# Kernel optimization log

Measured on AMD Instinct MI355X. Metric: run time of the kernel, lower is better.

## Reference

```python
import jax, jax.numpy as jnp
from jax import lax
import numpy as np

# correlation hyperparams (from init_kwargs)
MAX_D = 32      # maxDisplacement
PAD = 1         # zero padding
K = 3           # patch (kernel) size
STRIDE_K = 1    # stride over output pixels
STRIDE_D = 1    # stride over displacements


def setup_inputs() -> dict:
    key = jax.random.key(0)
    k0, k1 = jax.random.split(key)
    x0 = jax.random.normal(k0, (4, 64, 256, 512), dtype=jnp.float32)
    x1 = jax.random.normal(k1, (4, 64, 256, 512), dtype=jnp.float32)
    return {"x0": x0, "x1": x1}


def _corr2d(x0, x1):
    # x0, x1: [B, C, H, W] NCHW feature maps
    B, C, H, W = x0.shape
    # zero-pad spatially; x1 gets extra width padding so all displacements are in-bounds
    x0p = jnp.pad(x0, ((0, 0), (0, 0), (PAD, PAD), (PAD, PAD)))
    x1p = jnp.pad(x1, ((0, 0), (0, 0), (PAD, PAD), (PAD + MAX_D, PAD + MAX_D)))
    Wp = W + 2 * PAD
    # width offsets into x1p for displacements d = -MAX_D .. MAX_D step STRIDE_D
    offsets = jnp.arange(0, 2 * MAX_D + 1, STRIDE_D, dtype=jnp.int32)

    def step(carry, off):
        x1s = lax.dynamic_slice_in_dim(x1p, off, Wp, axis=3)   # [B,C,Hp,Wp]
        prod = jnp.sum(x0p * x1s, axis=1)                      # channel dot -> [B,Hp,Wp]
        # KxK box-sum over the patch, stride STRIDE_K -> [B,Ho,Wo]
        s = lax.reduce_window(prod, jnp.float32(0), lax.add,
                              (1, K, K), (1, STRIDE_K, STRIDE_K), 'VALID')
        return carry, s

    _, out = lax.scan(step, None, offsets)        # [nD, B, Ho, Wo]
    out = jnp.transpose(out, (1, 0, 2, 3))        # [B, nD, Ho, Wo]
    return out / jnp.asarray(K * K * C, out.dtype)


def reference(x0, x1):
    return _corr2d(x0, x1)
```

## Files before the change

### kernel.cpp

```cpp
#include <hip/hip_runtime.h>

#define WF 512
#define HF 256
#define CF 64
#define NDTOT 65
#define DP 72

static constexpr size_t CH  = (size_t)HF * WF;
static constexpr size_t WH  = (size_t)HF * WF;
static constexpr float  INV = 1.0f / 576.0f;

typedef _Float16 f16;
typedef _Float16 f16x4 __attribute__((ext_vector_type(4)));
typedef _Float16 f16x8 __attribute__((ext_vector_type(8)));
typedef float    f32x4 __attribute__((ext_vector_type(4)));

#if __has_builtin(__builtin_amdgcn_mfma_f32_16x16x16f16)
#define MFMA16(A, B, C) __builtin_amdgcn_mfma_f32_16x16x16f16((A), (B), (C), 0, 0, 0)
#define FRAG_T f16x4
__device__ __forceinline__ f16x4 mkfrag(f16 a, f16 b, f16 c, f16 d) {
    f16x4 r; r[0] = a; r[1] = b; r[2] = c; r[3] = d; return r;
}
#else
#define MFMA16(A, B, C) __builtin_amdgcn_mfma_f32_16x16x32_f16((A), (B), (C), 0, 0, 0)
#define FRAG_T f16x8
__device__ __forceinline__ f16x8 mkfrag(f16 a, f16 b, f16 c, f16 d) {
    f16x8 r; r[0] = a; r[1] = b; r[2] = c; r[3] = d;
    r[4] = (f16)0.f; r[5] = (f16)0.f; r[6] = (f16)0.f; r[7] = (f16)0.f; return r;
}
#endif

#define GLOADF(dst, ptr, offbytes) \
    asm volatile("global_load_dword %0, %1, %2" \
                 : "=v"(dst) : "v"(offbytes), "s"(ptr))

__global__ __launch_bounds__(256) __attribute__((amdgpu_waves_per_eu(3)))
void corr_gram(const float* __restrict__ x0, const float* __restrict__ x1,
               f16* __restrict__ ws) {
    const int f = blockIdx.x;
    const int tid = (f & 7) * 512 + (f >> 3);
    const int b = tid >> 10;
    const int y = (tid >> 2) & 255;
    const int sg = tid & 3;

    const int t = threadIdx.x;
    const int l = t & 63;
    const int w = t >> 6;
    const int xs = (sg * 4 + w) * 32;
    const int jb = xs - 32;

    const int n  = l & 15;
    const int kq = l >> 4;

    __shared__ f16 ebs[4][2304];

    const float* x0r = x0 + (size_t)b * CF * CH + (size_t)y * WF;
    const float* x1r = x1 + (size_t)b * CF * CH + (size_t)y * WF;

    int aB[2];
#pragma unroll
    for (int xt = 0; xt < 2; ++xt)
        aB[xt] = (4 * kq * (int)CH + xs + 16 * xt + n) * 4;
    int bB[6]; bool okj[6];
#pragma unroll
    for (int jt = 0; jt < 6; ++jt) {
        int col = jb + 16 * jt + n;
        okj[jt] = (unsigned)col < (unsigned)WF;
        col = col < 0 ? 0 : (col > 511 ? 511 : col);
        bB[jt] = (4 * kq * (int)CH + col) * 4;
    }

    f32x4 acc[10];
#pragma unroll
    for (int i = 0; i < 10; ++i) acc[i] = (f32x4)0.0f;

    float bufs[8][8];
    FRAG_T ah0, ah1, al0, al1;

#define ISS_A(kk, B) do { \
    _Pragma("unroll") for (int xt = 0; xt < 2; ++xt) \
    _Pragma("unroll") for (int i = 0; i < 4; ++i) \
        GLOADF(bufs[B][4*xt+i], x0r, aB[xt] + (16*(kk)+i) * (int)(CH*4)); \
    __builtin_amdgcn_sched_barrier(0); \
} while (0)

#define ISS_B(kk, p, B) do { \
    _Pragma("unroll") for (int u = 0; u < 2; ++u) \
    _Pragma("unroll") for (int i = 0; i < 4; ++i) \
        GLOADF(bufs[B][4*u+i], x1r, bB[2*((p)-1)+u] + (16*(kk)+i) * (int)(CH*4)); \
    __builtin_amdgcn_sched_barrier(0); \
} while (0)

#define WAITN(N) do { asm volatile("s_waitcnt vmcnt(" #N ")" ::: "memory"); \
                      __builtin_amdgcn_sched_barrier(0); } while (0)

#define TRIPLE(ai, AH, AL) do { \
    acc[ai] = MFMA16(AH, bh, acc[ai]); \
    acc[ai] = MFMA16(AH, bl, acc[ai]); \
    acc[ai] = MFMA16(AL, bh, acc[ai]); } while (0)

#define CON_A(B) do { \
    { const float v0 = bufs[B][0], v1 = bufs[B][1], v2 = bufs[B][2], v3 = bufs[B][3]; \
      const f16 h0 = (f16)v0, h1 = (f16)v1, h2 = (f16)v2, h3 = (f16)v3; \
      ah0 = mkfrag(h0, h1, h2, h3); \
      al0 = mkfrag((f16)(v0-(float)h0), (f16)(v1-(float)h1), (f16)(v2-(float)h2), (f16)(v3-(float)h3)); } \
    { const float v0 = bufs[B][4], v1 = bufs[B][5], v2 = bufs[B][6], v3 = bufs[B][7]; \
      const f16 h0 = (f16)v0, h1 = (f16)v1, h2 = (f16)v2, h3 = (f16)v3; \
      ah1 = mkfrag(h0, h1, h2, h3); \
      al1 = mkfrag((f16)(v0-(float)h0), (f16)(v1-(float)h1), (f16)(v2-(float)h2), (f16)(v3-(float)h3)); } \
} while (0)

#define CON_B(p, B) do { \
    _Pragma("unroll") for (int u = 0; u < 2; ++u) { \
        const int jt = 2*((p)-1) + u; \
        float v0 = bufs[B][4*u], v1 = bufs[B][4*u+1], v2 = bufs[B][4*u+2], v3 = bufs[B][4*u+3]; \
        v0 = okj[jt] ? v0 : 0.f; v1 = okj[jt] ? v1 : 0.f; \
        v2 = okj[jt] ? v2 : 0.f; v3 = okj[jt] ? v3 : 0.f; \
        const f16 h0 = (f16)v0, h1 = (f16)v1, h2 = (f16)v2, h3 = (f16)v3; \
        const FRAG_T bh = mkfrag(h0, h1, h2, h3); \
        const FRAG_T bl = mkfrag((f16)(v0-(float)h0), (f16)(v1-(float)h1), \
                                 (f16)(v2-(float)h2), (f16)(v3-(float)h3)); \
        if (jt < 5)  TRIPLE(jt, ah0, al0); \
        if (jt >= 1) TRIPLE(4 + jt, ah1, al1); \
    } \
} while (0)

    ISS_A(0, 0); ISS_B(0, 1, 1); ISS_B(0, 2, 2); ISS_B(0, 3, 3);
    ISS_A(1, 4); ISS_B(1, 1, 5); ISS_B(1, 2, 6);

    WAITN(48); ISS_B(1, 3, 7); CON_A(0);
    WAITN(48); ISS_A(2, 0);    CON_B(1, 1);
    WAITN(48); ISS_B(2, 1, 1); CON_B(2, 2);
    WAITN(48); ISS_B(2, 2, 2); CON_B(3, 3);
    WAITN(48); ISS_B(2, 3, 3); CON_A(4);
    WAITN(48); ISS_A(3, 4);    CON_B(1, 5);
    WAITN(48); ISS_B(3, 1, 5); CON_B(2, 6);
    WAITN(48); ISS_B(3, 2, 6); CON_B(3, 7);
    WAITN(48); ISS_B(3, 3, 7); CON_A(0);
    WAITN(48); CON_B(1, 1);
    WAITN(40); CON_B(2, 2);
    WAITN(32); CON_B(3, 3);
    WAITN(24); CON_A(4);
    WAITN(16); CON_B(1, 5);
    WAITN(8);  CON_B(2, 6);
    WAITN(0);  CON_B(3, 7);

#undef CON_B
#undef CON_A
#undef TRIPLE
#undef WAITN
#undef ISS_B
#undef ISS_A

    f16* eb = ebs[w];
#pragma unroll
    for (int xt = 0; xt < 2; ++xt) {
#pragma unroll
        for (int p = 0; p < 5; ++p) {
            const int i = xt * 5 + p;
#pragma unroll
            for (int q = 0; q < 4; ++q) {
                const int m = kq * 4 + q;
                const int xl = xt * 16 + m;
                const int d = 16 * p + n - m;
                if ((unsigned)d < (unsigned)NDTOT)
                    eb[xl * DP + d] = (f16)acc[i][q];
            }
        }
    }
#pragma unroll
    for (int i = 0; i < 4; ++i) {
        const int idx = l + 64 * i;
        if (idx < 224) {
            const int xl = idx / 7;
            eb[xl * DP + NDTOT + (idx - 7 * xl)] = (f16)0.f;
        }
    }
    uint4* dst = (uint4*)(ws + ((size_t)(b * HF + y) * WF + xs) * DP);
    const uint4* src = (const uint4*)eb;
#pragma unroll
    for (int i = 0; i < 5; ++i) {
        const int idx = l + 64 * i;
        if (idx < 288) dst[idx] = src[idx];
    }
}

__global__ __launch_bounds__(256)
void corr_box(const f16* __restrict__ ws, float* __restrict__ out) {
    const int xt = blockIdx.x;
    const int yt = blockIdx.y;
    const int b = blockIdx.z;
    const int t = threadIdx.x;
    const int x0b = xt * 32, y0 = yt * 8;

    __shared__ f16 S[10 * 34][DP];

    for (int u = 0; u < 10; ++u) {
        const int yy = y0 - 1 + u;
        const bool yok = (unsigned)yy < (unsigned)HF;
        const f16* src = ws + ((size_t)(b * HF + yy) * WF + (x0b - 1)) * DP;
#pragma unroll
        for (int sub = 0; sub < 2; ++sub) {
            const int idx = sub * 256 + t;
            if (idx < 306) {
                const int v = idx / 9, dg = idx - v * 9;
                const int xx = x0b - 1 + v;
                f16x8 val;
#pragma unroll
                for (int jj = 0; jj < 8; ++jj) val[jj] = (f16)0.f;
                if (yok && (unsigned)xx < (unsigned)WF)
                    val = *(const f16x8*)(src + (size_t)v * DP + dg * 8);
                *(f16x8*)&S[u * 34 + v][dg * 8] = val;
            }
        }
    }
    __syncthreads();

    const int ly = t >> 5, lx = t & 31;
    const int yg = y0 + ly, xg = x0b + lx;
    float* o0 = out + (size_t)b * NDTOT * WH + (size_t)yg * WF + xg;

#pragma unroll 1
    for (int dg = 0; dg < 9; ++dg) {
        f16x8 s;
#pragma unroll
        for (int jj = 0; jj < 8; ++jj) s[jj] = (f16)0.f;
#pragma unroll
        for (int du = 0; du < 3; ++du)
#pragma unroll
            for (int dv = 0; dv < 3; ++dv)
                s += *(const f16x8*)&S[(ly + du) * 34 + (lx + dv)][dg * 8];
#pragma unroll
        for (int jj = 0; jj < 8; ++jj) {
            const int d = dg * 8 + jj;
            if (d < NDTOT) o0[(size_t)d * WH] = (float)s[jj] * INV;
        }
    }
}

__global__ void corr_naive(const float* __restrict__ x0, const float* __restrict__ x1,
                           float* __restrict__ out) {
    const size_t total = (size_t)4 * NDTOT * WH;
    size_t idx = (size_t)blockIdx.x * blockDim.x + threadIdx.x;
    if (idx >= total) return;
    const int j = (int)(idx % WF);
    const int i = (int)((idx / WF) % HF);
    const int d = (int)((idx / WH) % NDTOT);
    const int b = (int)(idx / ((size_t)NDTOT * WH));
    const int disp = d - 32;
    float s = 0.f;
    for (int u = i - 1; u <= i + 1; ++u) {
        if (u < 0 || u >= HF) continue;
        for (int v = j - 1; v <= j + 1; ++v) {
            if (v < 0 || v >= WF) continue;
            const int v1c = v + disp;
            if (v1c < 0 || v1c >= WF) continue;
            const float* p0 = x0 + (size_t)b * CF * CH + (size_t)u * WF + v;
            const float* p1 = x1 + (size_t)b * CF * CH + (size_t)u * WF + v1c;
            for (int c = 0; c < CF; ++c)
                s += p0[(size_t)c * CH] * p1[(size_t)c * CH];
        }
    }
    out[idx] = s * INV;
}

extern "C" void kernel_launch(void* const* d_in, const int* in_sizes, int n_in,
                              void* d_out, int out_size, void* d_ws, size_t ws_size,
                              hipStream_t stream) {
    const float* x0 = (const float*)d_in[0];
    const float* x1 = (const float*)d_in[1];
    float* out = (float*)d_out;

    const size_t wsNeed = (size_t)4 * HF * WF * DP * sizeof(f16);

    if (ws_size >= wsNeed) {
        f16* ws = (f16*)d_ws;
        corr_gram<<<dim3(4096), dim3(256), 0, stream>>>(x0, x1, ws);
        corr_box<<<dim3(16, 32, 4), dim3(256), 0, stream>>>(ws, out);
    } else {
        const size_t total = (size_t)4 * NDTOT * WH;
        const int blocks = (int)((total + 255) / 256);
        corr_naive<<<dim3(blocks), dim3(256), 0, stream>>>(x0, x1, out);
    }
}
```

Before: 133.0 us.

## Stage operand loads through LDS with global_load_lds instead of register dword loads

Replaces the per-lane scalar global_load_dword register pipeline, which had many loads in flight across 8 register buffers, with 16-byte global_load_lds transfers straight into a per-wave LDS tile. Fragments are then read back from LDS. Each of the 4 channel chunks is issued once and prefetched one step ahead of compute. The aim is fewer, wider memory instructions and lower register pressure, and the occupancy hint rises from 3 to 4-8 waves per EU. The trade-off is an extra LDS round trip and a shallower prefetch, with a full vmcnt(0) wait each step.

```diff
diff --git a/kernel.cpp b/kernel.cpp
--- a/kernel.cpp
+++ b/kernel.cpp
@@ -14,6 +14,9 @@
 typedef _Float16 f16x4 __attribute__((ext_vector_type(4)));
 typedef _Float16 f16x8 __attribute__((ext_vector_type(8)));
 typedef float    f32x4 __attribute__((ext_vector_type(4)));
+
+typedef __attribute__((address_space(3))) void lds_void_t;
+typedef const __attribute__((address_space(1))) void glb_void_t;
 
 #if __has_builtin(__builtin_amdgcn_mfma_f32_16x16x16f16)
 #define MFMA16(A, B, C) __builtin_amdgcn_mfma_f32_16x16x16f16((A), (B), (C), 0, 0, 0)
@@ -30,11 +33,7 @@
 }
 #endif
 
-#define GLOADF(dst, ptr, offbytes) \
-    asm volatile("global_load_dword %0, %1, %2" \
-                 : "=v"(dst) : "v"(offbytes), "s"(ptr))
-
-__global__ __launch_bounds__(256) __attribute__((amdgpu_waves_per_eu(3)))
+__global__ __launch_bounds__(256) __attribute__((amdgpu_waves_per_eu(4, 8)))
 void corr_gram(const float* __restrict__ x0, const float* __restrict__ x1,
                f16* __restrict__ ws) {
     const int f = blockIdx.x;
@@ -52,68 +51,80 @@
     const int n  = l & 15;
     const int kq = l >> 4;
 
-    __shared__ f16 ebs[4][2304];
+    __shared__ float lds[8192];
+    const int wbase = w * 2048;
 
     const float* x0r = x0 + (size_t)b * CF * CH + (size_t)y * WF;
     const float* x1r = x1 + (size_t)b * CF * CH + (size_t)y * WF;
 
-    int aB[2];
-#pragma unroll
-    for (int xt = 0; xt < 2; ++xt)
-        aB[xt] = (4 * kq * (int)CH + xs + 16 * xt + n) * 4;
-    int bB[6]; bool okj[6];
-#pragma unroll
-    for (int jt = 0; jt < 6; ++jt) {
-        int col = jb + 16 * jt + n;
-        okj[jt] = (unsigned)col < (unsigned)WF;
-        col = col < 0 ? 0 : (col > 511 ? 511 : col);
-        bB[jt] = (4 * kq * (int)CH + col) * 4;
-    }
+    const int offA0 = (l >> 3) * (int)CH + xs + 4 * (l & 7);
+    const int offA1 = offA0 + 8 * (int)CH;
+    int offB[6];
+#pragma unroll
+    for (int r = 0; r < 6; ++r) {
+        const int P = r * 64 + l;
+        const int ch = P / 24;
+        const int rem = P - 24 * ch;
+        int col = jb + 4 * rem;
+        col = col < 0 ? 0 : (col > 508 ? 508 : col);
+        offB[r] = ch * (int)CH + col;
+    }
+
+    const int fA = wbase + kq * 128 + n;
+    const int fB = wbase + 512 + kq * 384 + n;
+
+    bool okj[6];
+#pragma unroll
+    for (int jt = 0; jt < 6; ++jt) okj[jt] = (unsigned)(jb + 16 * jt + n) < (unsigned)WF;
 
     f32x4 acc[10];
 #pragma unroll
     for (int i = 0; i < 10; ++i) acc[i] = (f32x4)0.0f;
 
-    float bufs[8][8];
-    FRAG_T ah0, ah1, al0, al1;
-
-#define ISS_A(kk, B) do { \
-    _Pragma("unroll") for (int xt = 0; xt < 2; ++xt) \
-    _Pragma("unroll") for (int i = 0; i < 4; ++i) \
-        GLOADF(bufs[B][4*xt+i], x0r, aB[xt] + (16*(kk)+i) * (int)(CH*4)); \
-    __builtin_amdgcn_sched_barrier(0); \
+#define ISSUE(kk) do { \
+    const float* x0k = x0r + (size_t)(kk) * 16 * CH; \
+    const float* x1k = x1r + (size_t)(kk) * 16 * CH; \
+    __builtin_amdgcn_global_load_lds((glb_void_t*)(x0k + offA0), (lds_void_t*)(lds + wbase),       16, 0, 0); \
+    __builtin_amdgcn_global_load_lds((glb_void_t*)(x0k + offA1), (lds_void_t*)(lds + wbase + 256), 16, 0, 0); \
+    _Pragma("unroll") \
+    for (int r = 0; r < 6; ++r) \
+        __builtin_amdgcn_global_load_lds((glb_void_t*)(x1k + offB[r]), \
+            (lds_void_t*)(lds + wbase + 512 + r * 256), 16, 0, 0); \
 } while (0)
-
-#define ISS_B(kk, p, B) do { \
-    _Pragma("unroll") for (int u = 0; u < 2; ++u) \
-    _Pragma("unroll") for (int i = 0; i < 4; ++i) \
-        GLOADF(bufs[B][4*u+i], x1r, bB[2*((p)-1)+u] + (16*(kk)+i) * (int)(CH*4)); \
-    __builtin_amdgcn_sched_barrier(0); \
-} while (0)
-
-#define WAITN(N) do { asm volatile("s_waitcnt vmcnt(" #N ")" ::: "memory"); \
-                      __builtin_amdgcn_sched_barrier(0); } while (0)
 
 #define TRIPLE(ai, AH, AL) do { \
     acc[ai] = MFMA16(AH, bh, acc[ai]); \
     acc[ai] = MFMA16(AH, bl, acc[ai]); \
     acc[ai] = MFMA16(AL, bh, acc[ai]); } while (0)
 
-#define CON_A(B) do { \
-    { const float v0 = bufs[B][0], v1 = bufs[B][1], v2 = bufs[B][2], v3 = bufs[B][3]; \
+#define COMPUTE(kk) do { \
+    asm volatile("s_waitcnt vmcnt(0)" ::: "memory"); \
+    __builtin_amdgcn_sched_barrier(0); \
+    float fa[2][4], fb[6][4]; \
+    _Pragma("unroll") \
+    for (int xt = 0; xt < 2; ++xt) \
+    _Pragma("unroll") \
+    for (int i = 0; i < 4; ++i) fa[xt][i] = lds[fA + i * 32 + xt * 16]; \
+    _Pragma("unroll") \
+    for (int jt = 0; jt < 6; ++jt) \
+    _Pragma("unroll") \
+    for (int i = 0; i < 4; ++i) fb[jt][i] = lds[fB + i * 96 + jt * 16]; \
+    asm volatile("s_waitcnt lgkmcnt(0)" ::: "memory"); \
+    __builtin_amdgcn_sched_barrier(0); \
+    if ((kk) < 3) ISSUE((kk) + 1); \
+    __builtin_amdgcn_sched_barrier(0); \
+    FRAG_T ah0, al0, ah1, al1; \
+    { const float v0 = fa[0][0], v1 = fa[0][1], v2 = fa[0][2], v3 = fa[0][3]; \
       const f16 h0 = (f16)v0, h1 = (f16)v1, h2 = (f16)v2, h3 = (f16)v3; \
       ah0 = mkfrag(h0, h1, h2, h3); \
       al0 = mkfrag((f16)(v0-(float)h0), (f16)(v1-(float)h1), (f16)(v2-(float)h2), (f16)(v3-(float)h3)); } \
-    { const float v0 = bufs[B][4], v1 = bufs[B][5], v2 = bufs[B][6], v3 = bufs[B][7]; \
+    { const float v0 = fa[1][0], v1 = fa[1][1], v2 = fa[1][2], v3 = fa[1][3]; \
       const f16 h0 = (f16)v0, h1 = (f16)v1, h2 = (f16)v2, h3 = (f16)v3; \
       ah1 = mkfrag(h0, h1, h2, h3); \
       al1 = mkfrag((f16)(v0-(float)h0), (f16)(v1-(float)h1), (f16)(v2-(float)h2), (f16)(v3-(float)h3)); } \
-} while (0)
-
-#define CON_B(p, B) do { \
-    _Pragma("unroll") for (int u = 0; u < 2; ++u) { \
-        const int jt = 2*((p)-1) + u; \
-        float v0 = bufs[B][4*u], v1 = bufs[B][4*u+1], v2 = bufs[B][4*u+2], v3 = bufs[B][4*u+3]; \
+    _Pragma("unroll") \
+    for (int jt = 0; jt < 6; ++jt) { \
+        float v0 = fb[jt][0], v1 = fb[jt][1], v2 = fb[jt][2], v3 = fb[jt][3]; \
         v0 = okj[jt] ? v0 : 0.f; v1 = okj[jt] ? v1 : 0.f; \
         v2 = okj[jt] ? v2 : 0.f; v3 = okj[jt] ? v3 : 0.f; \
         const f16 h0 = (f16)v0, h1 = (f16)v1, h2 = (f16)v2, h3 = (f16)v3; \
@@ -125,34 +136,17 @@
     } \
 } while (0)
 
-    ISS_A(0, 0); ISS_B(0, 1, 1); ISS_B(0, 2, 2); ISS_B(0, 3, 3);
-    ISS_A(1, 4); ISS_B(1, 1, 5); ISS_B(1, 2, 6);
-
-    WAITN(48); ISS_B(1, 3, 7); CON_A(0);
-    WAITN(48); ISS_A(2, 0);    CON_B(1, 1);
-    WAITN(48); ISS_B(2, 1, 1); CON_B(2, 2);
-    WAITN(48); ISS_B(2, 2, 2); CON_B(3, 3);
-    WAITN(48); ISS_B(2, 3, 3); CON_A(4);
-    WAITN(48); ISS_A(3, 4);    CON_B(1, 5);
-    WAITN(48); ISS_B(3, 1, 5); CON_B(2, 6);
-    WAITN(48); ISS_B(3, 2, 6); CON_B(3, 7);
-    WAITN(48); ISS_B(3, 3, 7); CON_A(0);
-    WAITN(48); CON_B(1, 1);
-    WAITN(40); CON_B(2, 2);
-    WAITN(32); CON_B(3, 3);
-    WAITN(24); CON_A(4);
-    WAITN(16); CON_B(1, 5);
-    WAITN(8);  CON_B(2, 6);
-    WAITN(0);  CON_B(3, 7);
-
-#undef CON_B
-#undef CON_A
+    ISSUE(0);
+    COMPUTE(0);
+    COMPUTE(1);
+    COMPUTE(2);
+    COMPUTE(3);
+
+#undef COMPUTE
 #undef TRIPLE
-#undef WAITN
-#undef ISS_B
-#undef ISS_A
-
-    f16* eb = ebs[w];
+#undef ISSUE
+
+    f16* eb = (f16*)(lds + wbase);
 #pragma unroll
     for (int xt = 0; xt < 2; ++xt) {
 #pragma unroll
```

Result: faster. 128.8 us (-3.2%).
